# Kernel optimization log

Measured on AMD Instinct MI355X. Metric: run time of the kernel, lower is better.

## Reference

```python
import jax, jax.numpy as jnp
import numpy as np

RADIUS_IN = 0.05
RADIUS_OUT = 0.2
NSAMPLE = 32


def setup_inputs() -> dict:
    key = jax.random.key(0)
    k1, k2, k3 = jax.random.split(key, 3)
    B, N, M, C = 2, 16384, 2048, 64
    xyz = jax.random.uniform(k1, (B, N, 3), dtype=jnp.float32)
    new_xyz = jax.random.uniform(k2, (B, M, 3), dtype=jnp.float32)
    features = jax.random.normal(k3, (B, C, N), dtype=jnp.float32)
    return {"xyz": xyz, "new_xyz": new_xyz, "features": features}


def _ball_query_dilated(xyz, new_xyz, r_in, r_out, nsample):
    # xyz: (B,N,3), new_xyz: (B,M,3)
    d2 = jnp.sum((new_xyz[:, :, None, :] - xyz[:, None, :, :]) ** 2, axis=-1)  # (B,M,N)
    mask = (d2 >= r_in * r_in) & (d2 < r_out * r_out)  # dilated shell
    B, M, N = mask.shape
    rank = jnp.cumsum(mask, axis=-1) - 1  # order of each match along N
    cnt = jnp.minimum(jnp.sum(mask, axis=-1), nsample).astype(jnp.int32)  # (B,M)
    # scatter the j-th point index into slot `rank` (overflow slots dumped into pad)
    pos = jnp.where(mask & (rank < nsample), rank, nsample)
    b = jnp.arange(B)[:, None, None]
    m = jnp.arange(M)[None, :, None]
    j = jnp.broadcast_to(jnp.arange(N, dtype=jnp.int32)[None, None, :], (B, M, N))
    idx = jnp.zeros((B, M, nsample + 1), jnp.int32).at[b, m, pos].set(j)[..., :nsample]
    # CUDA kernel fills unused slots with the FIRST matched index (0 if no match)
    slot = jnp.arange(nsample)[None, None, :]
    idx = jnp.where(slot < cnt[..., None], idx, idx[..., :1])
    return cnt, idx


def _group(features, idx):
    # features: (B,C,N), idx: (B,M,S) -> (B,C,M,S)
    B, C, N = features.shape
    _, M, S = idx.shape
    flat = idx.reshape(B, 1, M * S)
    return jnp.take_along_axis(features, flat, axis=2).reshape(B, C, M, S)


def reference(xyz, new_xyz, features):
    idx_cnt, idx = _ball_query_dilated(xyz, new_xyz, RADIUS_IN, RADIUS_OUT, NSAMPLE)
    xyz_t = jnp.transpose(xyz, (0, 2, 1))            # (B,3,N)
    grouped_xyz = _group(xyz_t, idx)                 # (B,3,M,S)
    grouped_xyz = grouped_xyz - jnp.transpose(new_xyz, (0, 2, 1))[..., None]
    grouped_features = _group(features, idx)         # (B,C,M,S)
    new_features = jnp.concatenate([grouped_xyz, grouped_features], axis=1)
    return idx_cnt, new_features
```

## Files before the change

kernel.cpp:

```cpp
#include <hip/hip_runtime.h>
#include <cstdint>

#define BB 2
#define NN 16384
#define MM 2048
#define CC 64
#define SS 32
#define NWAVE 8
#define SEG (NN / NWAVE)

__device__ __forceinline__ float dist2(float qx, float qy, float qz,
                                       float px, float py, float pz) {
    float dx = __fsub_rn(qx, px), dy = __fsub_rn(qy, py), dz = __fsub_rn(qz, pz);
    return __fadd_rn(__fadd_rn(__fmul_rn(dx, dx), __fmul_rn(dy, dy)), __fmul_rn(dz, dz));
}

__global__ __launch_bounds__(256) void transpose_feat(
    const float* __restrict__ f, float* __restrict__ ft) {
    __shared__ float tile[32][33];
    int bid = blockIdx.x;
    int n0 = (bid & 511) * 32;
    int c0 = ((bid >> 9) & 1) * 32;
    int b = bid >> 10;
    int tx = threadIdx.x & 31, ty = threadIdx.x >> 5;
#pragma unroll
    for (int k = 0; k < 32; k += 8)
        tile[ty + k][tx] = f[((size_t)(b * CC + c0 + ty + k)) * NN + n0 + tx];
    __syncthreads();
#pragma unroll
    for (int k = 0; k < 32; k += 8)
        ft[((size_t)(b * NN + n0 + ty + k)) * CC + c0 + tx] = tile[tx][ty + k];
}

__global__ __launch_bounds__(512) void qg_kernel(
    const float* __restrict__ xyz, const float* __restrict__ new_xyz,
    const float* __restrict__ feat_t, float* __restrict__ out) {
    constexpr float R_IN2 = 0.05f * 0.05f;
    constexpr float R_OUT2 = 0.2f * 0.2f;
    __shared__ int idxL[NWAVE][SS];
    __shared__ int cS[NWAVE];
    __shared__ int idxS[SS];
    __shared__ float fbuf[SS][CC + 4];

    int tid = threadIdx.x;
    int lane = tid & 63;
    int w = tid >> 6;
    int bm = blockIdx.x;
    int b = bm >> 11;
    int m = bm & 2047;

    float qx = new_xyz[(size_t)bm * 3 + 0];
    float qy = new_xyz[(size_t)bm * 3 + 1];
    float qz = new_xyz[(size_t)bm * 3 + 2];

    unsigned long long below = (1ull << lane) - 1ull;
    int c = 0;
    int base = w * SEG;
    for (int j0 = base; j0 < base + SEG; j0 += 256) {
        float px[4], py[4], pz[4];
        const float* pp = xyz + ((size_t)(b * NN + j0 + lane)) * 3;
#pragma unroll
        for (int u = 0; u < 4; ++u) {
            px[u] = pp[u * 192 + 0];
            py[u] = pp[u * 192 + 1];
            pz[u] = pp[u * 192 + 2];
        }
#pragma unroll
        for (int u = 0; u < 4; ++u) {
            float d2 = dist2(qx, qy, qz, px[u], py[u], pz[u]);
            bool inshell = (d2 >= R_IN2) && (d2 < R_OUT2);
            unsigned long long mk = __ballot(inshell);
            if (inshell) {
                int r = c + __popcll(mk & below);
                if (r < SS) idxL[w][r] = j0 + u * 64 + lane;
            }
            c += __popcll(mk);
        }
        if (c >= SS) break;
    }
    if (c > SS) c = SS;
    if (lane == 0) cS[w] = c;
    __syncthreads();

    if (tid < SS) {
        int r = tid;
        int acc = 0, pick = -1, off = 0;
#pragma unroll
        for (int s = 0; s < NWAVE; ++s) {
            int cs = cS[s];
            if (pick < 0 && r < acc + cs) { pick = s; off = r - acc; }
            acc += cs;
        }
        int cnt = acc < SS ? acc : SS;
        int j;
        if (r < cnt) {
            j = idxL[pick][off];
        } else {
            int s0 = -1;
#pragma unroll
            for (int s = 0; s < NWAVE; ++s)
                if (s0 < 0 && cS[s] > 0) s0 = s;
            j = (s0 >= 0) ? idxL[s0][0] : 0;
        }
        idxS[r] = j;
        if (r == 0) out[bm] = (float)cnt;
    }
    __syncthreads();

    float* gout = out + BB * MM;

    {
        int sl = tid >> 4, c4 = tid & 15;
        float4 v = ((const float4*)(feat_t + ((size_t)b * NN + idxS[sl]) * CC))[c4];
        *((float4*)&fbuf[sl][c4 * 4]) = v;
    }

    if (tid < 96) {
        int ch = tid >> 5, s = tid & 31;
        int j = idxS[s];
        float pv = xyz[((size_t)(b * NN) + j) * 3 + ch];
        float qv = new_xyz[(size_t)bm * 3 + ch];
        gout[((size_t)(b * 67 + ch) * MM + m) * SS + s] = __fsub_rn(pv, qv);
    }
    __syncthreads();

    {
        int ch = tid >> 3, sg = tid & 7;
        float4 v = make_float4(fbuf[sg * 4 + 0][ch], fbuf[sg * 4 + 1][ch],
                               fbuf[sg * 4 + 2][ch], fbuf[sg * 4 + 3][ch]);
        *((float4*)&gout[((size_t)(b * 67 + 3 + ch) * MM + m) * SS + sg * 4]) = v;
    }
}

__global__ __launch_bounds__(256) void query_group_fallback(
    const float* __restrict__ xyz, const float* __restrict__ new_xyz,
    const float* __restrict__ features, float* __restrict__ out) {
    constexpr float R_IN2 = 0.05f * 0.05f;
    constexpr float R_OUT2 = 0.2f * 0.2f;
    __shared__ int idxS[4][SS];

    int lane = threadIdx.x & 63;
    int w = threadIdx.x >> 6;
    int bm = blockIdx.x * 4 + w;
    int b = bm >> 11;
    int m = bm & 2047;

    float qx = new_xyz[(size_t)bm * 3 + 0];
    float qy = new_xyz[(size_t)bm * 3 + 1];
    float qz = new_xyz[(size_t)bm * 3 + 2];

    if (lane == 0) idxS[w][0] = 0;

    unsigned long long below = (1ull << lane) - 1ull;
    int cnt = 0;
    for (int j0 = 0; j0 < NN; j0 += 256) {
        float px[4], py[4], pz[4];
        const float* pp = xyz + ((size_t)(b * NN + j0 + lane)) * 3;
#pragma unroll
        for (int u = 0; u < 4; ++u) {
            px[u] = pp[u * 192 + 0];
            py[u] = pp[u * 192 + 1];
            pz[u] = pp[u * 192 + 2];
        }
#pragma unroll
        for (int u = 0; u < 4; ++u) {
            float d2 = dist2(qx, qy, qz, px[u], py[u], pz[u]);
            bool inshell = (d2 >= R_IN2) && (d2 < R_OUT2);
            unsigned long long mk = __ballot(inshell);
            if (inshell) {
                int r = cnt + __popcll(mk & below);
                if (r < SS) idxS[w][r] = j0 + u * 64 + lane;
            }
            cnt += __popcll(mk);
        }
        if (cnt >= SS) break;
    }
    if (cnt > SS) cnt = SS;
    if (lane == 0) out[bm] = (float)cnt;

    float* gout = out + BB * MM;
    int s = lane & 31, half = lane >> 5;
    int j = (s < cnt) ? idxS[w][s] : idxS[w][0];
    const float* pp = xyz + ((size_t)(b * NN) + j) * 3;
    float px = pp[0], py = pp[1], pz = pp[2];
    float v01 = half ? __fsub_rn(py, qy) : __fsub_rn(px, qx);
    gout[((size_t)(b * 67 + half) * MM + m) * SS + s] = v01;
    if (half == 0) gout[((size_t)(b * 67 + 2) * MM + m) * SS + s] = __fsub_rn(pz, qz);
#pragma unroll
    for (int k = 0; k < 32; ++k) {
        int ch = 2 * k + half;
        float v = features[((size_t)(b * CC + ch)) * NN + j];
        gout[((size_t)(b * 67 + 3 + ch) * MM + m) * SS + s] = v;
    }
}

extern "C" void kernel_launch(void* const* d_in, const int* in_sizes, int n_in,
                              void* d_out, int out_size, void* d_ws, size_t ws_size,
                              hipStream_t stream) {
    const float* xyz = (const float*)d_in[0];
    const float* new_xyz = (const float*)d_in[1];
    const float* features = (const float*)d_in[2];
    float* out = (float*)d_out;

    const size_t featT_bytes = (size_t)BB * NN * CC * 4;
    bool fast = ws_size >= featT_bytes;

    if (fast) {
        float* feat_t = (float*)d_ws;
        transpose_feat<<<2048, 256, 0, stream>>>(features, feat_t);
        qg_kernel<<<BB * MM, 512, 0, stream>>>(xyz, new_xyz, feat_t, out);
    } else {
        query_group_fallback<<<BB * MM / 4, 256, 0, stream>>>(xyz, new_xyz, features, out);
    }
}
```

Baseline: 104.2 us.

## Interleave ball-query chunks across waves with block-wide early termination

Instead of each wave scanning its own contiguous segment of the point cloud, waves now process interleaved 256-point chunks in lockstep steps. After each step a single thread accumulates per-chunk match counts, and the whole block stops once 32 neighbours are found. This removes the redundant scanning each wave did within its own segment, in exchange for two block barriers per step and a longer 64-chunk merge loop.

```diff
diff --git a/kernel.cpp b/kernel.cpp
--- a/kernel.cpp
+++ b/kernel.cpp
@@ -7,7 +7,8 @@
 #define CC 64
 #define SS 32
 #define NWAVE 8
-#define SEG (NN / NWAVE)
+#define NCH 64
+#define NSTEP 8
 
 __device__ __forceinline__ float dist2(float qx, float qy, float qz,
                                        float px, float py, float pz) {
@@ -37,8 +38,10 @@
     const float* __restrict__ feat_t, float* __restrict__ out) {
     constexpr float R_IN2 = 0.05f * 0.05f;
     constexpr float R_OUT2 = 0.2f * 0.2f;
-    __shared__ int idxL[NWAVE][SS];
-    __shared__ int cS[NWAVE];
+    __shared__ int idxC[NCH][SS];
+    __shared__ int cC[NCH];
+    __shared__ int sTotal;
+    __shared__ int sStop;
     __shared__ int idxS[SS];
     __shared__ float fbuf[SS][CC + 4];
 
@@ -53,10 +56,14 @@
     float qy = new_xyz[(size_t)bm * 3 + 1];
     float qz = new_xyz[(size_t)bm * 3 + 2];
 
+    if (tid < NCH) cC[tid] = 0;
+    if (tid == 0) { sTotal = 0; sStop = 0; }
+    __syncthreads();
+
     unsigned long long below = (1ull << lane) - 1ull;
-    int c = 0;
-    int base = w * SEG;
-    for (int j0 = base; j0 < base + SEG; j0 += 256) {
+    for (int t = 0; t < NSTEP; ++t) {
+        int ch = t * NWAVE + w;
+        int j0 = ch * 256;
         float px[4], py[4], pz[4];
         const float* pp = xyz + ((size_t)(b * NN + j0 + lane)) * 3;
 #pragma unroll
@@ -65,6 +72,7 @@
             py[u] = pp[u * 192 + 1];
             pz[u] = pp[u * 192 + 2];
         }
+        int c = 0;
 #pragma unroll
         for (int u = 0; u < 4; ++u) {
             float d2 = dist2(qx, qy, qz, px[u], py[u], pz[u]);
@@ -72,36 +80,36 @@
             unsigned long long mk = __ballot(inshell);
             if (inshell) {
                 int r = c + __popcll(mk & below);
-                if (r < SS) idxL[w][r] = j0 + u * 64 + lane;
+                if (r < SS) idxC[ch][r] = j0 + u * 64 + lane;
             }
             c += __popcll(mk);
         }
-        if (c >= SS) break;
-    }
-    if (c > SS) c = SS;
-    if (lane == 0) cS[w] = c;
-    __syncthreads();
+        if (lane == 0) cC[ch] = c < SS ? c : SS;
+        __syncthreads();
+        if (tid == 0) {
+            int tot = sTotal;
+#pragma unroll
+            for (int k = 0; k < NWAVE; ++k) tot += cC[t * NWAVE + k];
+            sTotal = tot;
+            if (tot >= SS) sStop = 1;
+        }
+        __syncthreads();
+        if (sStop) break;
+    }
 
     if (tid < SS) {
         int r = tid;
-        int acc = 0, pick = -1, off = 0;
-#pragma unroll
-        for (int s = 0; s < NWAVE; ++s) {
-            int cs = cS[s];
-            if (pick < 0 && r < acc + cs) { pick = s; off = r - acc; }
+        int acc = 0, pick = -1, off = 0, s0 = -1;
+        for (int ch = 0; ch < NCH; ++ch) {
+            int cs = cC[ch];
+            if (pick < 0 && r < acc + cs) { pick = ch; off = r - acc; }
+            if (s0 < 0 && cs > 0) s0 = ch;
             acc += cs;
         }
         int cnt = acc < SS ? acc : SS;
         int j;
-        if (r < cnt) {
-            j = idxL[pick][off];
-        } else {
-            int s0 = -1;
-#pragma unroll
-            for (int s = 0; s < NWAVE; ++s)
-                if (s0 < 0 && cS[s] > 0) s0 = s;
-            j = (s0 >= 0) ? idxL[s0][0] : 0;
-        }
+        if (r < cnt) j = idxC[pick][off];
+        else j = (s0 >= 0) ? idxC[s0][0] : 0;
         idxS[r] = j;
         if (r == 0) out[bm] = (float)cnt;
     }
```

New measurement: 130.7 us. +25.4%, slower.

## Split ball query into single-wave prefix scan plus fallback completion kernel

Applied to the files above, without the earlier changes.

The old kernel gave each query 8 waves, each independently scanning its own 2048-point segment. A new first kernel uses one wave per query to scan only the first 2048 points, and fully groups any query that already finds 32 neighbours there. Queries that come up short save their partial count and indices to workspace. A second kernel then scans the remaining points with 8 waves per query and merges the results in order. This removes the redundant parallel scanning for the common case. The cost is an extra launch of mostly idle blocks and a larger workspace requirement.

```diff
diff --git a/kernel.cpp b/kernel.cpp
--- a/kernel.cpp
+++ b/kernel.cpp
@@ -6,8 +6,10 @@
 #define MM 2048
 #define CC 64
 #define SS 32
-#define NWAVE 8
-#define SEG (NN / NWAVE)
+#define PRE 2048
+#define SEG2 1792
+#define WPB 4
+
 
 __device__ __forceinline__ float dist2(float qx, float qy, float qz,
                                        float px, float py, float pz) {
@@ -32,20 +34,18 @@
         ft[((size_t)(b * NN + n0 + ty + k)) * CC + c0 + tx] = tile[tx][ty + k];
 }
 
-__global__ __launch_bounds__(512) void qg_kernel(
+__global__ __launch_bounds__(256) void k1_scan_group(
     const float* __restrict__ xyz, const float* __restrict__ new_xyz,
-    const float* __restrict__ feat_t, float* __restrict__ out) {
+    const float* __restrict__ feat_t, int* __restrict__ pcnt,
+    int* __restrict__ pidx, float* __restrict__ out) {
     constexpr float R_IN2 = 0.05f * 0.05f;
     constexpr float R_OUT2 = 0.2f * 0.2f;
-    __shared__ int idxL[NWAVE][SS];
-    __shared__ int cS[NWAVE];
-    __shared__ int idxS[SS];
-    __shared__ float fbuf[SS][CC + 4];
-
-    int tid = threadIdx.x;
-    int lane = tid & 63;
-    int w = tid >> 6;
-    int bm = blockIdx.x;
+    __shared__ int idxS[WPB][SS];
+    __shared__ float fbuf[WPB][SS][CC + 4];
+
+    int lane = threadIdx.x & 63;
+    int w = threadIdx.x >> 6;
+    int bm = blockIdx.x * WPB + w;
     int b = bm >> 11;
     int m = bm & 2047;
 
@@ -54,106 +54,8 @@
     float qz = new_xyz[(size_t)bm * 3 + 2];
 
     unsigned long long below = (1ull << lane) - 1ull;
-    int c = 0;
-    int base = w * SEG;
-    for (int j0 = base; j0 < base + SEG; j0 += 256) {
-        float px[4], py[4], pz[4];
-        const float* pp = xyz + ((size_t)(b * NN + j0 + lane)) * 3;
-#pragma unroll
-        for (int u = 0; u < 4; ++u) {
-            px[u] = pp[u * 192 + 0];
-            py[u] = pp[u * 192 + 1];
-            pz[u] = pp[u * 192 + 2];
-        }
-#pragma unroll
-        for (int u = 0; u < 4; ++u) {
-            float d2 = dist2(qx, qy, qz, px[u], py[u], pz[u]);
-            bool inshell = (d2 >= R_IN2) && (d2 < R_OUT2);
-            unsigned long long mk = __ballot(inshell);
-            if (inshell) {
-                int r = c + __popcll(mk & below);
-                if (r < SS) idxL[w][r] = j0 + u * 64 + lane;
-            }
-            c += __popcll(mk);
-        }
-        if (c >= SS) break;
-    }
-    if (c > SS) c = SS;
-    if (lane == 0) cS[w] = c;
-    __syncthreads();
-
-    if (tid < SS) {
-        int r = tid;
-        int acc = 0, pick = -1, off = 0;
-#pragma unroll
-        for (int s = 0; s < NWAVE; ++s) {
-            int cs = cS[s];
-            if (pick < 0 && r < acc + cs) { pick = s; off = r - acc; }
-            acc += cs;
-        }
-        int cnt = acc < SS ? acc : SS;
-        int j;
-        if (r < cnt) {
-            j = idxL[pick][off];
-        } else {
-            int s0 = -1;
-#pragma unroll
-            for (int s = 0; s < NWAVE; ++s)
-                if (s0 < 0 && cS[s] > 0) s0 = s;
-            j = (s0 >= 0) ? idxL[s0][0] : 0;
-        }
-        idxS[r] = j;
-        if (r == 0) out[bm] = (float)cnt;
-    }
-    __syncthreads();
-
-    float* gout = out + BB * MM;
-
-    {
-        int sl = tid >> 4, c4 = tid & 15;
-        float4 v = ((const float4*)(feat_t + ((size_t)b * NN + idxS[sl]) * CC))[c4];
-        *((float4*)&fbuf[sl][c4 * 4]) = v;
-    }
-
-    if (tid < 96) {
-        int ch = tid >> 5, s = tid & 31;
-        int j = idxS[s];
-        float pv = xyz[((size_t)(b * NN) + j) * 3 + ch];
-        float qv = new_xyz[(size_t)bm * 3 + ch];
-        gout[((size_t)(b * 67 + ch) * MM + m) * SS + s] = __fsub_rn(pv, qv);
-    }
-    __syncthreads();
-
-    {
-        int ch = tid >> 3, sg = tid & 7;
-        float4 v = make_float4(fbuf[sg * 4 + 0][ch], fbuf[sg * 4 + 1][ch],
-                               fbuf[sg * 4 + 2][ch], fbuf[sg * 4 + 3][ch]);
-        *((float4*)&gout[((size_t)(b * 67 + 3 + ch) * MM + m) * SS + sg * 4]) = v;
-    }
-}
-
-__global__ __launch_bounds__(256) void query_group_fallback(
-    const float* __restrict__ xyz, const float* __restrict__ new_xyz,
-    const float* __restrict__ features, float* __restrict__ out) {
-    constexpr float R_IN2 = 0.05f * 0.05f;
-    constexpr float R_OUT2 = 0.2f * 0.2f;
-    __shared__ int idxS[4][SS];
-
-    int lane = threadIdx.x & 63;
-    int w = threadIdx.x >> 6;
-    int bm = blockIdx.x * 4 + w;
-    int b = bm >> 11;
-    int m = bm & 2047;
-
-    float qx = new_xyz[(size_t)bm * 3 + 0];
-    float qy = new_xyz[(size_t)bm * 3 + 1];
-    float qz = new_xyz[(size_t)bm * 3 + 2];
-
-    if (lane == 0) idxS[w][0] = 0;
-
-    unsigned long long below = (1ull << lane) - 1ull;
     int cnt = 0;
-    for (int j0 = 0; j0 < NN; j0 += 256) {
+    for (int j0 = 0; j0 < PRE; j0 += 256) {
         float px[4], py[4], pz[4];
         const float* pp = xyz + ((size_t)(b * NN + j0 + lane)) * 3;
 #pragma unroll
@@ -175,6 +77,198 @@
         }
         if (cnt >= SS) break;
     }
+    bool complete = cnt >= SS;
+    if (cnt > SS) cnt = SS;
+
+    if (!complete) {
+        if (lane == 0) pcnt[bm] = cnt;
+        if (lane < cnt) pidx[bm * SS + lane] = idxS[w][lane];
+        return;
+    }
+
+    if (lane == 0) { pcnt[bm] = SS; out[bm] = 32.0f; }
+
+    float* gout = out + BB * MM;
+
+    {
+        int s4 = lane >> 4, c4 = lane & 15;
+        int jj[8];
+#pragma unroll
+        for (int it = 0; it < 8; ++it) jj[it] = idxS[w][it * 4 + s4];
+        float4 vv[8];
+#pragma unroll
+        for (int it = 0; it < 8; ++it)
+            vv[it] = ((const float4*)(feat_t + ((size_t)b * NN + jj[it]) * CC))[c4];
+#pragma unroll
+        for (int it = 0; it < 8; ++it)
+            *((float4*)&fbuf[w][it * 4 + s4][c4 * 4]) = vv[it];
+    }
+
+    {
+        int s = lane & 31, half = lane >> 5;
+        int j = idxS[w][s];
+        const float* pp = xyz + ((size_t)(b * NN) + j) * 3;
+        float px = pp[0], py = pp[1], pz = pp[2];
+        float v01 = half ? __fsub_rn(py, qy) : __fsub_rn(px, qx);
+        gout[((size_t)(b * 67 + half) * MM + m) * SS + s] = v01;
+        if (half == 0)
+            gout[((size_t)(b * 67 + 2) * MM + m) * SS + s] = __fsub_rn(pz, qz);
+    }
+
+    {
+        int ch8 = lane >> 3, sg = lane & 7;
+#pragma unroll
+        for (int it = 0; it < 8; ++it) {
+            int ch = it * 8 + ch8;
+            float4 v = make_float4(fbuf[w][sg * 4 + 0][ch], fbuf[w][sg * 4 + 1][ch],
+                                   fbuf[w][sg * 4 + 2][ch], fbuf[w][sg * 4 + 3][ch]);
+            *((float4*)&gout[((size_t)(b * 67 + 3 + ch) * MM + m) * SS + sg * 4]) = v;
+        }
+    }
+}
+
+__global__ __launch_bounds__(512) void k2_finish(
+    const float* __restrict__ xyz, const float* __restrict__ new_xyz,
+    const float* __restrict__ feat_t, const int* __restrict__ pcnt,
+    const int* __restrict__ pidx, float* __restrict__ out) {
+    constexpr float R_IN2 = 0.05f * 0.05f;
+    constexpr float R_OUT2 = 0.2f * 0.2f;
+    int bm = blockIdx.x;
+    int c0 = pcnt[bm];
+    if (c0 >= SS) return;
+
+    __shared__ int idxC[9][SS];
+    __shared__ int cC[9];
+    __shared__ int idxS[SS];
+    __shared__ float fbuf[SS][CC + 4];
+
+    int tid = threadIdx.x;
+    int lane = tid & 63;
+    int w = tid >> 6;
+    int b = bm >> 11;
+    int m = bm & 2047;
+
+    float qx = new_xyz[(size_t)bm * 3 + 0];
+    float qy = new_xyz[(size_t)bm * 3 + 1];
+    float qz = new_xyz[(size_t)bm * 3 + 2];
+
+    if (tid < c0) idxC[0][tid] = pidx[bm * SS + tid];
+    if (tid == 0) cC[0] = c0;
+
+    unsigned long long below = (1ull << lane) - 1ull;
+    int c = 0;
+    int base = PRE + w * SEG2;
+    for (int j0 = base; j0 < base + SEG2; j0 += 256) {
+        float px[4], py[4], pz[4];
+        const float* pp = xyz + ((size_t)(b * NN + j0 + lane)) * 3;
+#pragma unroll
+        for (int u = 0; u < 4; ++u) {
+            px[u] = pp[u * 192 + 0];
+            py[u] = pp[u * 192 + 1];
+            pz[u] = pp[u * 192 + 2];
+        }
+#pragma unroll
+        for (int u = 0; u < 4; ++u) {
+            float d2 = dist2(qx, qy, qz, px[u], py[u], pz[u]);
+            bool inshell = (d2 >= R_IN2) && (d2 < R_OUT2);
+            unsigned long long mk = __ballot(inshell);
+            if (inshell) {
+                int r = c + __popcll(mk & below);
+                if (r < SS) idxC[1 + w][r] = j0 + u * 64 + lane;
+            }
+            c += __popcll(mk);
+        }
+        if (c >= SS) break;
+    }
+    if (lane == 0) cC[1 + w] = c < SS ? c : SS;
+    __syncthreads();
+
+    if (tid < SS) {
+        int r = tid, acc = 0, pick = -1, off = 0, s0 = -1;
+#pragma unroll
+        for (int l = 0; l < 9; ++l) {
+            int cs = cC[l];
+            if (pick < 0 && r < acc + cs) { pick = l; off = r - acc; }
+            if (s0 < 0 && cs > 0) s0 = l;
+            acc += cs;
+        }
+        int cnt = acc < SS ? acc : SS;
+        int j;
+        if (r < cnt) j = idxC[pick][off];
+        else j = (s0 >= 0) ? idxC[s0][0] : 0;
+        idxS[r] = j;
+        if (r == 0) out[bm] = (float)cnt;
+    }
+    __syncthreads();
+
+    float* gout = out + BB * MM;
+
+    {
+        int sl = tid >> 4, c4 = tid & 15;
+        float4 v = ((const float4*)(feat_t + ((size_t)b * NN + idxS[sl]) * CC))[c4];
+        *((float4*)&fbuf[sl][c4 * 4]) = v;
+    }
+
+    if (tid < 96) {
+        int ch = tid >> 5, s = tid & 31;
+        int j = idxS[s];
+        float pv = xyz[((size_t)(b * NN) + j) * 3 + ch];
+        float qv = new_xyz[(size_t)bm * 3 + ch];
+        gout[((size_t)(b * 67 + ch) * MM + m) * SS + s] = __fsub_rn(pv, qv);
+    }
+    __syncthreads();
+
+    {
+        int ch = tid >> 3, sg = tid & 7;
+        float4 v = make_float4(fbuf[sg * 4 + 0][ch], fbuf[sg * 4 + 1][ch],
+                               fbuf[sg * 4 + 2][ch], fbuf[sg * 4 + 3][ch]);
+        *((float4*)&gout[((size_t)(b * 67 + 3 + ch) * MM + m) * SS + sg * 4]) = v;
+    }
+}
+
+__global__ __launch_bounds__(256) void query_group_fallback(
+    const float* __restrict__ xyz, const float* __restrict__ new_xyz,
+    const float* __restrict__ features, float* __restrict__ out) {
+    constexpr float R_IN2 = 0.05f * 0.05f;
+    constexpr float R_OUT2 = 0.2f * 0.2f;
+    __shared__ int idxS[4][SS];
+
+    int lane = threadIdx.x & 63;
+    int w = threadIdx.x >> 6;
+    int bm = blockIdx.x * 4 + w;
+    int b = bm >> 11;
+    int m = bm & 2047;
+
+    float qx = new_xyz[(size_t)bm * 3 + 0];
+    float qy = new_xyz[(size_t)bm * 3 + 1];
+    float qz = new_xyz[(size_t)bm * 3 + 2];
+
+    if (lane == 0) idxS[w][0] = 0;
+
+    unsigned long long below = (1ull << lane) - 1ull;
+    int cnt = 0;
+    for (int j0 = 0; j0 < NN; j0 += 256) {
+        float px[4], py[4], pz[4];
+        const float* pp = xyz + ((size_t)(b * NN + j0 + lane)) * 3;
+#pragma unroll
+        for (int u = 0; u < 4; ++u) {
+            px[u] = pp[u * 192 + 0];
+            py[u] = pp[u * 192 + 1];
+            pz[u] = pp[u * 192 + 2];
+        }
+#pragma unroll
+        for (int u = 0; u < 4; ++u) {
+            float d2 = dist2(qx, qy, qz, px[u], py[u], pz[u]);
+            bool inshell = (d2 >= R_IN2) && (d2 < R_OUT2);
+            unsigned long long mk = __ballot(inshell);
+            if (inshell) {
+                int r = cnt + __popcll(mk & below);
+                if (r < SS) idxS[w][r] = j0 + u * 64 + lane;
+            }
+            cnt += __popcll(mk);
+        }
+        if (cnt >= SS) break;
+    }
     if (cnt > SS) cnt = SS;
     if (lane == 0) out[bm] = (float)cnt;
 
@@ -203,12 +297,17 @@
     float* out = (float*)d_out;
 
     const size_t featT_bytes = (size_t)BB * NN * CC * 4;
-    bool fast = ws_size >= featT_bytes;
+    const size_t pidx_bytes = (size_t)BB * MM * SS * 4;
+    const size_t pcnt_bytes = (size_t)BB * MM * 4;
+    bool fast = ws_size >= featT_bytes + pidx_bytes + pcnt_bytes;
 
     if (fast) {
         float* feat_t = (float*)d_ws;
+        int* pidx = (int*)((char*)d_ws + featT_bytes);
+        int* pcnt = (int*)((char*)d_ws + featT_bytes + pidx_bytes);
         transpose_feat<<<2048, 256, 0, stream>>>(features, feat_t);
-        qg_kernel<<<BB * MM, 512, 0, stream>>>(xyz, new_xyz, feat_t, out);
+        k1_scan_group<<<BB * MM / WPB, 256, 0, stream>>>(xyz, new_xyz, feat_t, pcnt, pidx, out);
+        k2_finish<<<BB * MM, 512, 0, stream>>>(xyz, new_xyz, feat_t, pcnt, pidx, out);
     } else {
         query_group_fallback<<<BB * MM / 4, 256, 0, stream>>>(xyz, new_xyz, features, out);
     }
```

New measurement: 94.89 us. -8.9%, faster.
